# Optimization experiments

Hardware: AMD Instinct MI355X
Metric: run time of the kernel (lower is better)

## Reference

```python
import jax, jax.numpy as jnp
import numpy as np
from jax import lax

MAX_FEATURES = 50000
WIDTH = 256
EMBED = 2 * WIDTH
NUM_CLASS = 2
BATCH = 64
SEQ = 512


def setup_inputs() -> dict:
    key = jax.random.key(0)
    ks = jax.random.split(key, 10)
    s = lambda *shape: 1.0 / np.sqrt(shape[0])
    tokens = jax.random.randint(ks[0], (BATCH, SEQ), 0, MAX_FEATURES, dtype=jnp.int32)
    emb = jax.random.normal(ks[1], (MAX_FEATURES, EMBED), jnp.float32) * 0.05
    W1 = jax.random.normal(ks[2], (EMBED, WIDTH), jnp.float32) * s(EMBED)
    U1 = jax.random.normal(ks[3], (WIDTH, WIDTH), jnp.float32) * s(WIDTH)
    b1 = jnp.zeros((WIDTH,), jnp.float32)
    W2 = jax.random.normal(ks[4], (WIDTH, WIDTH), jnp.float32) * s(WIDTH)
    U2 = jax.random.normal(ks[5], (WIDTH, WIDTH), jnp.float32) * s(WIDTH)
    b2 = jnp.zeros((WIDTH,), jnp.float32)
    Wd = jax.random.normal(ks[6], (WIDTH, NUM_CLASS), jnp.float32) * s(WIDTH)
    bd = jnp.zeros((NUM_CLASS,), jnp.float32)
    return {"tokens": tokens, "emb": emb, "W1": W1, "U1": U1, "b1": b1,
            "W2": W2, "U2": U2, "b2": b2, "Wd": Wd, "bd": bd}


def _simple_rnn(x, W, U, b, return_sequences):
    # x: [B, S, D] -> precompute input projection once (big GEMM), then scan
    B = x.shape[0]
    H = U.shape[0]
    xw = jnp.einsum('bsd,dh->bsh', x, W) + b  # [B, S, H]
    def step(h, xt):
        h_new = jnp.tanh(xt + h @ U)
        return h_new, h_new
    h0 = jnp.zeros((B, H), x.dtype)
    h_last, hs = lax.scan(step, h0, jnp.swapaxes(xw, 0, 1))  # hs: [S, B, H]
    if return_sequences:
        return jnp.swapaxes(hs, 0, 1)  # [B, S, H]
    return h_last  # [B, H]


def reference(tokens, emb, W1, U1, b1, W2, U2, b2, Wd, bd):
    x = emb[tokens]                                  # [B, S, 2W] embedding lookup
    h1 = _simple_rnn(x, W1, U1, b1, return_sequences=True)   # [B, S, W]
    h2 = _simple_rnn(h1, W2, U2, b2, return_sequences=False)  # [B, W]
    logits = h2 @ Wd + bd                            # [B, num_class]
    return jax.nn.softmax(logits, axis=-1)
```

## Files before the change

kernel.cpp:

```cpp
#include <hip/hip_runtime.h>

typedef __attribute__((ext_vector_type(8))) short bf16x8;
typedef __attribute__((ext_vector_type(4))) float f32x4;

static __device__ __forceinline__ unsigned short f2bf(float x) {
    unsigned int u = __float_as_uint(x);
    u += 0x7fffu + ((u >> 16) & 1u);
    return (unsigned short)(u >> 16);
}

static __device__ __forceinline__ float selq(const f32x4* a, int q) {
    return (q == 0) ? a[0][0] : (q == 1) ? a[1][0] : (q == 2) ? a[2][0] : a[3][0];
}

static __device__ __forceinline__ void barrier_lds_only() {
    __asm__ volatile("s_waitcnt lgkmcnt(0)\n\ts_barrier" ::: "memory");
}

__global__ void transpose4(const float* __restrict__ s0, const float* __restrict__ s1,
                           const float* __restrict__ s2, const float* __restrict__ s3,
                           unsigned short* __restrict__ d0, unsigned short* __restrict__ d1,
                           unsigned short* __restrict__ d2, unsigned short* __restrict__ d3) {
    int which = blockIdx.y;
    const float* src = which == 0 ? s0 : which == 1 ? s1 : which == 2 ? s2 : s3;
    unsigned short* dst = which == 0 ? d0 : which == 1 ? d1 : which == 2 ? d2 : d3;
    int K = (which == 0) ? 512 : 256;
    int idx = blockIdx.x * 256 + threadIdx.x;
    if (idx >= K * 256) return;
    int k = idx >> 8;
    int n = idx & 255;
    dst[n * K + k] = f2bf(src[idx]);
}

template<bool GATHER>
__global__ __launch_bounds__(256, 4) void gemm_mfma(
    const void* __restrict__ Aptr, const int* __restrict__ tokens,
    const unsigned short* __restrict__ Bt, const float* __restrict__ bias,
    float* __restrict__ C, int M, int N, int K)
{
    const int bn0 = blockIdx.x * 64;
    const int m0  = blockIdx.y * 64;
    const int tid = threadIdx.x;

    __shared__ unsigned short As[64 * 40];
    __shared__ unsigned short Bs[64 * 40];
    __shared__ int tok[64];

    const int r  = tid >> 2;
    const int c0 = (tid & 3) * 8;
    const int w  = tid >> 6;
    const int L  = tid & 63;
    const int ml = L & 15;
    const int q  = L >> 4;
    const int kq = q * 8;

    if (GATHER) {
        if (tid < 64) tok[tid] = tokens[m0 + tid];
        __syncthreads();
    }

    const float* af32 = nullptr;
    const unsigned short* abf = nullptr;
    if (GATHER) af32 = (const float*)Aptr + (size_t)tok[r] * K + c0;
    else        abf  = (const unsigned short*)Aptr + (size_t)(m0 + r) * K + c0;
    const unsigned short* bsrc = Bt + (size_t)(bn0 + r) * K + c0;

    float4 f0, f1; uint4 ab, bb;
    if (GATHER) { f0 = *(const float4*)af32; f1 = *(const float4*)(af32 + 4); af32 += 32; }
    else        { ab = *(const uint4*)abf; abf += 32; }
    bb = *(const uint4*)bsrc; bsrc += 32;

    f32x4 acc[4] = {};

    for (int k0 = 0; k0 < K; k0 += 32) {
        unsigned short tmp[8];
        if (GATHER) {
            tmp[0]=f2bf(f0.x); tmp[1]=f2bf(f0.y); tmp[2]=f2bf(f0.z); tmp[3]=f2bf(f0.w);
            tmp[4]=f2bf(f1.x); tmp[5]=f2bf(f1.y); tmp[6]=f2bf(f1.z); tmp[7]=f2bf(f1.w);
        } else {
            *(uint4*)tmp = ab;
        }
        *(uint4*)&As[r * 40 + c0] = *(const uint4*)tmp;
        *(uint4*)&Bs[r * 40 + c0] = bb;
        __syncthreads();

        if (k0 + 32 < K) {
            if (GATHER) { f0 = *(const float4*)af32; f1 = *(const float4*)(af32 + 4); af32 += 32; }
            else        { ab = *(const uint4*)abf; abf += 32; }
            bb = *(const uint4*)bsrc; bsrc += 32;
        }

        bf16x8 av = *(const bf16x8*)&As[(16 * w + ml) * 40 + kq];
#pragma unroll
        for (int ns = 0; ns < 4; ++ns) {
            bf16x8 bv = *(const bf16x8*)&Bs[(ns * 16 + ml) * 40 + kq];
            acc[ns] = __builtin_amdgcn_mfma_f32_16x16x32_bf16(av, bv, acc[ns], 0, 0, 0);
        }
        __syncthreads();
    }

#pragma unroll
    for (int ns = 0; ns < 4; ++ns) {
        int gn = bn0 + ns * 16 + ml;
        float bv = bias[gn];
#pragma unroll
        for (int rr = 0; rr < 4; ++rr) {
            int gm = m0 + 16 * w + q * 4 + rr;
            C[(size_t)gm * N + gn] = acc[ns][rr] + bv;
        }
    }
}

__global__ __launch_bounds__(512) void rnn_pipe(
    float* xw,
    const unsigned short* __restrict__ U1t,
    const unsigned short* __restrict__ W2t,
    const unsigned short* __restrict__ U2t,
    const float* __restrict__ b2,
    int* flags,
    float* __restrict__ out_last)
{
    const int bid = blockIdx.x;
    const int tid = threadIdx.x;
    const int w   = tid >> 6;
    const int rw  = w & 3;
    const int L   = tid & 63;
    const int col = tid & 255;
    const int q   = L >> 4;
    const int ml  = L & 15;

    __shared__ unsigned short ring[32][256];

    if (bid < 64) {
        const int b = bid;
        int* flagp = flags + b;

        bf16x8 Bf[4][8];
        const unsigned short* Bsrc = (w < 4) ? U1t : W2t;
#pragma unroll
        for (int i = 0; i < 4; ++i) {
            const unsigned short* up = Bsrc + (size_t)((rw * 4 + i) * 16 + ml) * 256 + q * 8;
#pragma unroll
            for (int kt = 0; kt < 8; ++kt)
                Bf[i][kt] = *(const bf16x8*)(up + kt * 32);
        }
        if (tid < 256) ring[31][tid] = 0;

        const float* xpf = xw + (size_t)b * 512 * 256 + col;
        float xq[4];
        float b2v[4];
        if (w < 4) {
            xq[0] = xpf[0]; xq[1] = xpf[256]; xq[2] = xpf[512]; xq[3] = xpf[768];
            xpf += 4 * 256;
        } else {
#pragma unroll
            for (int i = 0; i < 4; ++i) b2v[i] = b2[rw * 64 + i * 16 + ml];
        }
        float* pb = xw + (size_t)b * 512 * 256;
        __syncthreads();

        for (int g = 0; g < 32; ++g) {
            const int half = g & 1;
#pragma unroll
            for (int j = 0; j < 16; ++j) {
                if (w < 4) {
                    const int slot_r = (j == 0) ? ((half ^ 1) * 16 + 15) : (half * 16 + j - 1);
                    bf16x8 af[8];
#pragma unroll
                    for (int kt = 0; kt < 8; ++kt)
                        af[kt] = *(const bf16x8*)&ring[slot_r][kt * 32 + q * 8];
                    float xnew = *xpf; xpf += 256;
                    f32x4 accA[4] = {}, accB[4] = {};
#pragma unroll
                    for (int kt = 0; kt < 8; kt += 2) {
#pragma unroll
                        for (int i = 0; i < 4; ++i)
                            accA[i] = __builtin_amdgcn_mfma_f32_16x16x32_bf16(af[kt], Bf[i][kt], accA[i], 0, 0, 0);
#pragma unroll
                        for (int i = 0; i < 4; ++i)
                            accB[i] = __builtin_amdgcn_mfma_f32_16x16x32_bf16(af[kt + 1], Bf[i][kt + 1], accB[i], 0, 0, 0);
                    }
                    float z  = selq(accA, q) + selq(accB, q) + xq[j & 3];
                    float e  = __expf(2.f * z);
                    float hn = 1.f - 2.f * __builtin_amdgcn_rcpf(e + 1.f);
                    ring[half * 16 + j][col] = f2bf(hn);
                    xq[j & 3] = xnew;
                } else {
                    if (j == 0 && g > 0) {
                        const int half2 = half ^ 1;
                        const int t0 = (g - 1) * 16;
                        bf16x8 af[8];
#pragma unroll
                        for (int kt = 0; kt < 8; ++kt)
                            af[kt] = *(const bf16x8*)&ring[half2 * 16 + ml][kt * 32 + q * 8];
                        f32x4 acc[4] = {};
#pragma unroll
                        for (int kt = 0; kt < 8; ++kt)
#pragma unroll
                            for (int i = 0; i < 4; ++i)
                                acc[i] = __builtin_amdgcn_mfma_f32_16x16x32_bf16(af[kt], Bf[i][kt], acc[i], 0, 0, 0);
                        float* ps = pb + (size_t)t0 * 256 + q * 1024 + rw * 64 + ml;
#pragma unroll
                        for (int i = 0; i < 4; ++i)
#pragma unroll
                            for (int rr = 0; rr < 4; ++rr)
                                ps[rr * 256 + i * 16] = acc[i][rr] + b2v[i];
                    }
                    if (j == 8 && g > 0)
                        asm volatile("s_waitcnt vmcnt(0)" ::: "memory");
                }
                if (j == 9 && g > 0 && tid == 0)
                    __hip_atomic_store(flagp, 16 * g, __ATOMIC_RELEASE, __HIP_MEMORY_SCOPE_AGENT);
                barrier_lds_only();
            }
        }
        if (w >= 4) {
            bf16x8 af[8];
#pragma unroll
            for (int kt = 0; kt < 8; ++kt)
                af[kt] = *(const bf16x8*)&ring[16 + ml][kt * 32 + q * 8];
            f32x4 acc[4] = {};
#pragma unroll
            for (int kt = 0; kt < 8; ++kt)
#pragma unroll
                for (int i = 0; i < 4; ++i)
                    acc[i] = __builtin_amdgcn_mfma_f32_16x16x32_bf16(af[kt], Bf[i][kt], acc[i], 0, 0, 0);
            float* ps = pb + (size_t)496 * 256 + q * 1024 + rw * 64 + ml;
#pragma unroll
            for (int i = 0; i < 4; ++i)
#pragma unroll
                for (int rr = 0; rr < 4; ++rr)
                    ps[rr * 256 + i * 16] = acc[i][rr] + b2v[i];
            asm volatile("s_waitcnt vmcnt(0)" ::: "memory");
        }
        __builtin_amdgcn_s_barrier();
        if (tid == 0)
            __hip_atomic_store(flagp, 512, __ATOMIC_RELEASE, __HIP_MEMORY_SCOPE_AGENT);

    } else {
        const int b = bid - 64;
        int* flagp = flags + b;
        unsigned short (*hsh)[256] = ring;

        bf16x8 Bf[4][8];
#pragma unroll
        for (int i = 0; i < 4; ++i) {
            const unsigned short* up = U2t + (size_t)((rw * 4 + i) * 16 + ml) * 256 + q * 8;
#pragma unroll
            for (int kt = 0; kt < 8; ++kt)
                Bf[i][kt] = *(const bf16x8*)(up + kt * 32);
        }
        if (tid < 256) hsh[0][tid] = 0;
        const float* pbc = xw + (size_t)b * 512 * 256 + col;
        float lastv = 0.f;
        __syncthreads();

#define CTICK(RP, PV)                                                                \
    {                                                                                \
        if (w < 4) {                                                                 \
            bf16x8 af[8];                                                            \
            _Pragma("unroll")                                                        \
            for (int kt = 0; kt < 8; ++kt)                                           \
                af[kt] = *(const bf16x8*)&hsh[RP][kt * 32 + q * 8];                  \
            f32x4 accA[4] = {}, accB[4] = {};                                        \
            _Pragma("unroll")                                                        \
            for (int kt = 0; kt < 8; kt += 2) {                                      \
                _Pragma("unroll")                                                    \
                for (int i = 0; i < 4; ++i)                                          \
                    accA[i] = __builtin_amdgcn_mfma_f32_16x16x32_bf16(af[kt], Bf[i][kt], accA[i], 0, 0, 0);       \
                _Pragma("unroll")                                                    \
                for (int i = 0; i < 4; ++i)                                          \
                    accB[i] = __builtin_amdgcn_mfma_f32_16x16x32_bf16(af[kt + 1], Bf[i][kt + 1], accB[i], 0, 0, 0); \
            }                                                                        \
            float z  = selq(accA, q) + selq(accB, q) + (PV);                         \
            float e  = __expf(2.f * z);                                              \
            float hn = 1.f - 2.f * __builtin_amdgcn_rcpf(e + 1.f);                   \
            lastv = hn;                                                              \
            hsh[(RP) ^ 1][col] = f2bf(hn);                                           \
        }                                                                            \
        barrier_lds_only();                                                          \
    }

        for (int c = 0; c < 32; ++c) {
            const int t0 = c * 16;
            if (tid == 0) {
                int it = 0;
                while (__hip_atomic_load(flagp, __ATOMIC_ACQUIRE, __HIP_MEMORY_SCOPE_AGENT) < t0 + 16) {
                    __builtin_amdgcn_s_sleep(2);
                    if (++it > (1 << 17)) break;
                }
            }
            __syncthreads();
            float pv[16];
            if (w < 4) {
#pragma unroll
                for (int j = 0; j < 16; ++j)
                    pv[j] = pbc[(size_t)(t0 + j) << 8];
            }
            CTICK(0, pv[0])  CTICK(1, pv[1])  CTICK(0, pv[2])  CTICK(1, pv[3])
            CTICK(0, pv[4])  CTICK(1, pv[5])  CTICK(0, pv[6])  CTICK(1, pv[7])
            CTICK(0, pv[8])  CTICK(1, pv[9])  CTICK(0, pv[10]) CTICK(1, pv[11])
            CTICK(0, pv[12]) CTICK(1, pv[13]) CTICK(0, pv[14]) CTICK(1, pv[15])
        }
#undef CTICK

        if (w < 4) out_last[b * 256 + col] = lastv;
    }
}

__global__ void head_kernel(const float* __restrict__ h2, const float* __restrict__ Wd,
                            const float* __restrict__ bd, float* __restrict__ out)
{
    int tid = threadIdx.x;
    int b = tid >> 1, c = tid & 1;
    float s = bd[c];
    for (int jj = 0; jj < 256; ++jj) s = fmaf(h2[b * 256 + jj], Wd[jj * 2 + c], s);
    __shared__ float lg[128];
    lg[tid] = s;
    __syncthreads();
    float o0 = lg[b * 2 + 0], o1 = lg[b * 2 + 1];
    float m = fmaxf(o0, o1);
    float z = __expf(o0 - m) + __expf(o1 - m);
    out[tid] = __expf(s - m) * __builtin_amdgcn_rcpf(z);
}

extern "C" void kernel_launch(void* const* d_in, const int* in_sizes, int n_in,
                              void* d_out, int out_size, void* d_ws, size_t ws_size,
                              hipStream_t stream) {
    const int*   tokens = (const int*)d_in[0];
    const float* emb    = (const float*)d_in[1];
    const float* W1     = (const float*)d_in[2];
    const float* U1     = (const float*)d_in[3];
    const float* b1     = (const float*)d_in[4];
    const float* W2     = (const float*)d_in[5];
    const float* U2     = (const float*)d_in[6];
    const float* b2     = (const float*)d_in[7];
    const float* Wd     = (const float*)d_in[8];
    const float* bd     = (const float*)d_in[9];
    float* out = (float*)d_out;

    char* ws = (char*)d_ws;
    float*          xw  = (float*)ws;
    char*           p   = ws + 33554432 + 16777216;
    unsigned short* W1t = (unsigned short*)p;            p += 512 * 256 * 2;
    unsigned short* W2t = (unsigned short*)p;            p += 256 * 256 * 2;
    unsigned short* U1t = (unsigned short*)p;            p += 256 * 256 * 2;
    unsigned short* U2t = (unsigned short*)p;            p += 256 * 256 * 2;
    float*          h2  = (float*)p;                     p += 64 * 256 * 4;
    int*            flags = (int*)p;

    const int M = 64 * 512;

    hipMemsetAsync(flags, 0, 64 * sizeof(int), stream);

    transpose4<<<dim3(512, 4), 256, 0, stream>>>(W1, W2, U1, U2, W1t, W2t, U1t, U2t);

    gemm_mfma<true><<<dim3(256 / 64, M / 64), 256, 0, stream>>>(
        emb, tokens, W1t, b1, xw, M, 256, 512);

    rnn_pipe<<<128, 512, 0, stream>>>(xw, U1t, W2t, U2t, b2, flags, h2);

    head_kernel<<<1, 128, 0, stream>>>(h2, Wd, bd, out);
}
```

Before: 547.4 us.

## Shrink RNN pipeline blocks to 256 threads and stream W2 from memory

The layer-1 producer blocks drop from 512 threads (4 recurrence waves plus 4 waves holding W2 in registers) to 256 threads. The same waves now run both the recurrence and the per-chunk W2 projection. W2 fragments are reloaded from global memory every chunk instead of staying in registers, and a partial vmcnt wait replaces the full wait. The consumer blocks also shrink to 256 threads by removing the idle waves. This aims to cut barrier cost and wasted waves per step, but it puts the W2 GEMV and its global loads on the critical recurrence path.

```diff
diff --git a/kernel.cpp b/kernel.cpp
--- a/kernel.cpp
+++ b/kernel.cpp
@@ -111,8 +111,9 @@
     }
 }
 
-__global__ __launch_bounds__(512) void rnn_pipe(
-    float* xw,
+__global__ __launch_bounds__(256, 1) void rnn_pipe(
+    const float* __restrict__ xw_in,
+    float* __restrict__ p_out,
     const unsigned short* __restrict__ U1t,
     const unsigned short* __restrict__ W2t,
     const unsigned short* __restrict__ U2t,
@@ -123,9 +124,8 @@
     const int bid = blockIdx.x;
     const int tid = threadIdx.x;
     const int w   = tid >> 6;
-    const int rw  = w & 3;
     const int L   = tid & 63;
-    const int col = tid & 255;
+    const int col = tid;
     const int q   = L >> 4;
     const int ml  = L & 15;
 
@@ -135,104 +135,103 @@
         const int b = bid;
         int* flagp = flags + b;
 
-        bf16x8 Bf[4][8];
-        const unsigned short* Bsrc = (w < 4) ? U1t : W2t;
+        bf16x8 U1f[4][8];
 #pragma unroll
         for (int i = 0; i < 4; ++i) {
-            const unsigned short* up = Bsrc + (size_t)((rw * 4 + i) * 16 + ml) * 256 + q * 8;
+            const unsigned short* up = U1t + (size_t)((w * 4 + i) * 16 + ml) * 256 + q * 8;
 #pragma unroll
             for (int kt = 0; kt < 8; ++kt)
-                Bf[i][kt] = *(const bf16x8*)(up + kt * 32);
-        }
-        if (tid < 256) ring[31][tid] = 0;
-
-        const float* xpf = xw + (size_t)b * 512 * 256 + col;
+                U1f[i][kt] = *(const bf16x8*)(up + kt * 32);
+        }
+        ring[31][tid] = 0;
+
+        const float* xpf = xw_in + (size_t)b * 512 * 256 + col;
         float xq[4];
+        xq[0] = xpf[0]; xq[1] = xpf[256]; xq[2] = xpf[512]; xq[3] = xpf[768];
+        xpf += 4 * 256;
         float b2v[4];
-        if (w < 4) {
-            xq[0] = xpf[0]; xq[1] = xpf[256]; xq[2] = xpf[512]; xq[3] = xpf[768];
-            xpf += 4 * 256;
-        } else {
-#pragma unroll
-            for (int i = 0; i < 4; ++i) b2v[i] = b2[rw * 64 + i * 16 + ml];
-        }
-        float* pb = xw + (size_t)b * 512 * 256;
-        __syncthreads();
+#pragma unroll
+        for (int i = 0; i < 4; ++i) b2v[i] = b2[w * 64 + i * 16 + ml];
+        float* pb = p_out + (size_t)b * 512 * 256;
+        const unsigned short* wbase = W2t + (size_t)((w * 4) * 16 + ml) * 256 + q * 8;
+        __syncthreads();
+
+#define GEMV_CHUNK(SRCH, T0)                                                         \
+    {                                                                                \
+        bf16x8 wf0[8], wf1[8], afg[8];                                               \
+        _Pragma("unroll")                                                            \
+        for (int kt = 0; kt < 8; ++kt) wf0[kt] = *(const bf16x8*)(wbase + kt * 32);  \
+        _Pragma("unroll")                                                            \
+        for (int kt = 0; kt < 8; ++kt) wf1[kt] = *(const bf16x8*)(wbase + 16 * 256 + kt * 32); \
+        _Pragma("unroll")                                                            \
+        for (int kt = 0; kt < 8; ++kt)                                               \
+            afg[kt] = *(const bf16x8*)&ring[(SRCH) * 16 + ml][kt * 32 + q * 8];      \
+        f32x4 ac0 = {}, ac1 = {}, ac2 = {}, ac3 = {};                                \
+        _Pragma("unroll")                                                            \
+        for (int kt = 0; kt < 8; ++kt)                                               \
+            ac0 = __builtin_amdgcn_mfma_f32_16x16x32_bf16(afg[kt], wf0[kt], ac0, 0, 0, 0); \
+        _Pragma("unroll")                                                            \
+        for (int kt = 0; kt < 8; ++kt) wf0[kt] = *(const bf16x8*)(wbase + 32 * 256 + kt * 32); \
+        _Pragma("unroll")                                                            \
+        for (int kt = 0; kt < 8; ++kt)                                               \
+            ac1 = __builtin_amdgcn_mfma_f32_16x16x32_bf16(afg[kt], wf1[kt], ac1, 0, 0, 0); \
+        _Pragma("unroll")                                                            \
+        for (int kt = 0; kt < 8; ++kt) wf1[kt] = *(const bf16x8*)(wbase + 48 * 256 + kt * 32); \
+        _Pragma("unroll")                                                            \
+        for (int kt = 0; kt < 8; ++kt)                                               \
+            ac2 = __builtin_amdgcn_mfma_f32_16x16x32_bf16(afg[kt], wf0[kt], ac2, 0, 0, 0); \
+        _Pragma("unroll")                                                            \
+        for (int kt = 0; kt < 8; ++kt)                                               \
+            ac3 = __builtin_amdgcn_mfma_f32_16x16x32_bf16(afg[kt], wf1[kt], ac3, 0, 0, 0); \
+        float* ps = pb + (size_t)(T0) * 256 + q * 1024 + w * 64 + ml;                \
+        _Pragma("unroll")                                                            \
+        for (int rr = 0; rr < 4; ++rr) {                                             \
+            ps[rr * 256 +  0] = ac0[rr] + b2v[0];                                    \
+            ps[rr * 256 + 16] = ac1[rr] + b2v[1];                                    \
+            ps[rr * 256 + 32] = ac2[rr] + b2v[2];                                    \
+            ps[rr * 256 + 48] = ac3[rr] + b2v[3];                                    \
+        }                                                                            \
+    }
 
         for (int g = 0; g < 32; ++g) {
             const int half = g & 1;
 #pragma unroll
             for (int j = 0; j < 16; ++j) {
-                if (w < 4) {
-                    const int slot_r = (j == 0) ? ((half ^ 1) * 16 + 15) : (half * 16 + j - 1);
-                    bf16x8 af[8];
-#pragma unroll
-                    for (int kt = 0; kt < 8; ++kt)
-                        af[kt] = *(const bf16x8*)&ring[slot_r][kt * 32 + q * 8];
-                    float xnew = *xpf; xpf += 256;
-                    f32x4 accA[4] = {}, accB[4] = {};
-#pragma unroll
-                    for (int kt = 0; kt < 8; kt += 2) {
-#pragma unroll
-                        for (int i = 0; i < 4; ++i)
-                            accA[i] = __builtin_amdgcn_mfma_f32_16x16x32_bf16(af[kt], Bf[i][kt], accA[i], 0, 0, 0);
-#pragma unroll
-                        for (int i = 0; i < 4; ++i)
-                            accB[i] = __builtin_amdgcn_mfma_f32_16x16x32_bf16(af[kt + 1], Bf[i][kt + 1], accB[i], 0, 0, 0);
-                    }
-                    float z  = selq(accA, q) + selq(accB, q) + xq[j & 3];
-                    float e  = __expf(2.f * z);
-                    float hn = 1.f - 2.f * __builtin_amdgcn_rcpf(e + 1.f);
-                    ring[half * 16 + j][col] = f2bf(hn);
-                    xq[j & 3] = xnew;
-                } else {
-                    if (j == 0 && g > 0) {
-                        const int half2 = half ^ 1;
-                        const int t0 = (g - 1) * 16;
-                        bf16x8 af[8];
-#pragma unroll
-                        for (int kt = 0; kt < 8; ++kt)
-                            af[kt] = *(const bf16x8*)&ring[half2 * 16 + ml][kt * 32 + q * 8];
-                        f32x4 acc[4] = {};
-#pragma unroll
-                        for (int kt = 0; kt < 8; ++kt)
-#pragma unroll
-                            for (int i = 0; i < 4; ++i)
-                                acc[i] = __builtin_amdgcn_mfma_f32_16x16x32_bf16(af[kt], Bf[i][kt], acc[i], 0, 0, 0);
-                        float* ps = pb + (size_t)t0 * 256 + q * 1024 + rw * 64 + ml;
-#pragma unroll
-                        for (int i = 0; i < 4; ++i)
-#pragma unroll
-                            for (int rr = 0; rr < 4; ++rr)
-                                ps[rr * 256 + i * 16] = acc[i][rr] + b2v[i];
-                    }
-                    if (j == 8 && g > 0)
-                        asm volatile("s_waitcnt vmcnt(0)" ::: "memory");
+                if (j == 0 && g > 0)
+                    GEMV_CHUNK(half ^ 1, (g - 1) * 16)
+                if (j == 8)
+                    asm volatile("s_waitcnt vmcnt(7)" ::: "memory");
+
+                const int slot_r = (j == 0) ? ((half ^ 1) * 16 + 15) : (half * 16 + j - 1);
+                bf16x8 af[8];
+#pragma unroll
+                for (int kt = 0; kt < 8; ++kt)
+                    af[kt] = *(const bf16x8*)&ring[slot_r][kt * 32 + q * 8];
+                float xnew = *xpf; xpf += 256;
+                f32x4 accA[4] = {}, accB[4] = {};
+#pragma unroll
+                for (int kt = 0; kt < 8; kt += 2) {
+#pragma unroll
+                    for (int i = 0; i < 4; ++i)
+                        accA[i] = __builtin_amdgcn_mfma_f32_16x16x32_bf16(af[kt], U1f[i][kt], accA[i], 0, 0, 0);
+#pragma unroll
+                    for (int i = 0; i < 4; ++i)
+                        accB[i] = __builtin_amdgcn_mfma_f32_16x16x32_bf16(af[kt + 1], U1f[i][kt + 1], accB[i], 0, 0, 0);
                 }
+                float z  = selq(accA, q) + selq(accB, q) + xq[j & 3];
+                float e  = __expf(2.f * z);
+                float hn = 1.f - 2.f * __builtin_amdgcn_rcpf(e + 1.f);
+                ring[half * 16 + j][col] = f2bf(hn);
+                xq[j & 3] = xnew;
+
                 if (j == 9 && g > 0 && tid == 0)
                     __hip_atomic_store(flagp, 16 * g, __ATOMIC_RELEASE, __HIP_MEMORY_SCOPE_AGENT);
                 barrier_lds_only();
             }
         }
-        if (w >= 4) {
-            bf16x8 af[8];
-#pragma unroll
-            for (int kt = 0; kt < 8; ++kt)
-                af[kt] = *(const bf16x8*)&ring[16 + ml][kt * 32 + q * 8];
-            f32x4 acc[4] = {};
-#pragma unroll
-            for (int kt = 0; kt < 8; ++kt)
-#pragma unroll
-                for (int i = 0; i < 4; ++i)
-                    acc[i] = __builtin_amdgcn_mfma_f32_16x16x32_bf16(af[kt], Bf[i][kt], acc[i], 0, 0, 0);
-            float* ps = pb + (size_t)496 * 256 + q * 1024 + rw * 64 + ml;
-#pragma unroll
-            for (int i = 0; i < 4; ++i)
-#pragma unroll
-                for (int rr = 0; rr < 4; ++rr)
-                    ps[rr * 256 + i * 16] = acc[i][rr] + b2v[i];
-            asm volatile("s_waitcnt vmcnt(0)" ::: "memory");
-        }
+        GEMV_CHUNK(1, 496)
+#undef GEMV_CHUNK
+        asm volatile("s_waitcnt vmcnt(0)" ::: "memory");
         __builtin_amdgcn_s_barrier();
         if (tid == 0)
             __hip_atomic_store(flagp, 512, __ATOMIC_RELEASE, __HIP_MEMORY_SCOPE_AGENT);
@@ -245,39 +244,37 @@
         bf16x8 Bf[4][8];
 #pragma unroll
         for (int i = 0; i < 4; ++i) {
-            const unsigned short* up = U2t + (size_t)((rw * 4 + i) * 16 + ml) * 256 + q * 8;
+            const unsigned short* up = U2t + (size_t)((w * 4 + i) * 16 + ml) * 256 + q * 8;
 #pragma unroll
             for (int kt = 0; kt < 8; ++kt)
                 Bf[i][kt] = *(const bf16x8*)(up + kt * 32);
         }
-        if (tid < 256) hsh[0][tid] = 0;
-        const float* pbc = xw + (size_t)b * 512 * 256 + col;
+        hsh[0][tid] = 0;
+        const float* pbc = p_out + (size_t)b * 512 * 256 + col;
         float lastv = 0.f;
         __syncthreads();
 
 #define CTICK(RP, PV)                                                                \
     {                                                                                \
-        if (w < 4) {                                                                 \
-            bf16x8 af[8];                                                            \
+        bf16x8 af[8];                                                                \
+        _Pragma("unroll")                                                            \
+        for (int kt = 0; kt < 8; ++kt)                                               \
+            af[kt] = *(const bf16x8*)&hsh[RP][kt * 32 + q * 8];                     \
+        f32x4 accA[4] = {}, accB[4] = {};                                            \
+        _Pragma("unroll")                                                            \
+        for (int kt = 0; kt < 8; kt += 2) {                                          \
             _Pragma("unroll")                                                        \
-            for (int kt = 0; kt < 8; ++kt)                                           \
-                af[kt] = *(const bf16x8*)&hsh[RP][kt * 32 + q * 8];                  \
-            f32x4 accA[4] = {}, accB[4] = {};                                        \
+            for (int i = 0; i < 4; ++i)                                              \
+                accA[i] = __builtin_amdgcn_mfma_f32_16x16x32_bf16(af[kt], Bf[i][kt], accA[i], 0, 0, 0);       \
             _Pragma("unroll")                                                        \
-            for (int kt = 0; kt < 8; kt += 2) {                                      \
-                _Pragma("unroll")                                                    \
-                for (int i = 0; i < 4; ++i)                                          \
-                    accA[i] = __builtin_amdgcn_mfma_f32_16x16x32_bf16(af[kt], Bf[i][kt], accA[i], 0, 0, 0);       \
-                _Pragma("unroll")                                                    \
-                for (int i = 0; i < 4; ++i)                                          \
-                    accB[i] = __builtin_amdgcn_mfma_f32_16x16x32_bf16(af[kt + 1], Bf[i][kt + 1], accB[i], 0, 0, 0); \
-            }                                                                        \
-            float z  = selq(accA, q) + selq(accB, q) + (PV);                         \
-            float e  = __expf(2.f * z);                                              \
-            float hn = 1.f - 2.f * __builtin_amdgcn_rcpf(e + 1.f);                   \
-            lastv = hn;                                                              \
-            hsh[(RP) ^ 1][col] = f2bf(hn);                                           \
+            for (int i = 0; i < 4; ++i)                                              \
+                accB[i] = __builtin_amdgcn_mfma_f32_16x16x32_bf16(af[kt + 1], Bf[i][kt + 1], accB[i], 0, 0, 0); \
         }                                                                            \
+        float z  = selq(accA, q) + selq(accB, q) + (PV);                             \
+        float e  = __expf(2.f * z);                                                  \
+        float hn = 1.f - 2.f * __builtin_amdgcn_rcpf(e + 1.f);                       \
+        lastv = hn;                                                                  \
+        hsh[(RP) ^ 1][col] = f2bf(hn);                                               \
         barrier_lds_only();                                                          \
     }
 
@@ -292,11 +289,9 @@
             }
             __syncthreads();
             float pv[16];
-            if (w < 4) {
-#pragma unroll
-                for (int j = 0; j < 16; ++j)
-                    pv[j] = pbc[(size_t)(t0 + j) << 8];
-            }
+#pragma unroll
+            for (int j = 0; j < 16; ++j)
+                pv[j] = pbc[(size_t)(t0 + j) << 8];
             CTICK(0, pv[0])  CTICK(1, pv[1])  CTICK(0, pv[2])  CTICK(1, pv[3])
             CTICK(0, pv[4])  CTICK(1, pv[5])  CTICK(0, pv[6])  CTICK(1, pv[7])
             CTICK(0, pv[8])  CTICK(1, pv[9])  CTICK(0, pv[10]) CTICK(1, pv[11])
@@ -304,7 +299,7 @@
         }
 #undef CTICK
 
-        if (w < 4) out_last[b * 256 + col] = lastv;
+        out_last[b * 256 + col] = lastv;
     }
 }
 
@@ -358,7 +353,7 @@
     gemm_mfma<true><<<dim3(256 / 64, M / 64), 256, 0, stream>>>(
         emb, tokens, W1t, b1, xw, M, 256, 512);
 
-    rnn_pipe<<<128, 512, 0, stream>>>(xw, U1t, W2t, U2t, b2, flags, h2);
+    rnn_pipe<<<128, 256, 0, stream>>>(xw, xw, U1t, W2t, U2t, b2, flags, h2);
 
     head_kernel<<<1, 128, 0, stream>>>(h2, Wd, bd, out);
 }
```

Measured after the change: 637.0 us. 1.16x slower.
